# Optimization experiments

Hardware: AMD Instinct MI355X
Metric: run time of the kernel (lower is better)

## Reference

```python
import jax, jax.numpy as jnp
import numpy as np

# Graph geometry: G complete graphs (molecules) of n nodes each.
N_PER_G, G, DEG = 64, 256, 16
H, D = 8, 8
IN_DIM = H * D      # 64
EDGE_DIM = 64
N = N_PER_G * G                      # 16384 nodes
EF = G * N_PER_G * N_PER_G           # 1,048,576 full edges
ES = G * N_PER_G * DEG               # 262,144 sparse edges
SCALE = float(np.sqrt(D))


def _edges():
    n = N_PER_G
    # full graph: all (i -> j) pairs per block, edge id = b*n*n + i*n + j
    ij = np.arange(n * n)
    i, j = ij // n, ij % n
    b = np.arange(G)[:, None]
    src_full = (b * n + i[None, :]).reshape(-1).astype(np.int32)
    dst_full = (b * n + j[None, :]).reshape(-1).astype(np.int32)
    # sparse graph: each dst j receives from DEG distinct sources (j+1..j+DEG mod n)
    jj = np.arange(n)[:, None]
    kk = np.arange(DEG)[None, :]
    ii = (jj + 1 + kk) % n
    eid_block = (ii * n + jj).reshape(-1)                 # [n*DEG]
    sparse_eid = (np.arange(G)[:, None] * n * n + eid_block[None, :]).reshape(-1).astype(np.int32)
    return jnp.asarray(src_full), jnp.asarray(dst_full), jnp.asarray(sparse_eid)


def setup_inputs() -> dict:
    key = jax.random.key(0)
    ks = jax.random.split(key, 16)
    w = lambda k, shape, s=0.05: s * jax.random.normal(k, shape, jnp.float32)
    src_full, dst_full, sparse_eid = _edges()
    return dict(
        h=jax.random.normal(ks[0], (N, IN_DIM), jnp.float32),
        e=jax.random.normal(ks[1], (ES, EDGE_DIM), jnp.float32),
        adj2=jax.random.uniform(ks[2], (EF,), jnp.float32),
        rel_pos_3d=jax.random.normal(ks[3], (EF, H), jnp.float32),
        Wq=w(ks[4], (H * D, IN_DIM)), bq=jnp.zeros((H * D,), jnp.float32),
        Wk=w(ks[5], (H * D, IN_DIM)), bk=jnp.zeros((H * D,), jnp.float32),
        Wv=w(ks[6], (H * D, IN_DIM)), bv=jnp.zeros((H * D,), jnp.float32),
        Wpe=w(ks[7], (H, EDGE_DIM)), bpe=jnp.zeros((H,), jnp.float32),
        Wap=w(ks[8], (EDGE_DIM, H)), bap=jnp.zeros((EDGE_DIM,), jnp.float32),
        Wo=w(ks[9], (H * D, H * D)), bo=jnp.zeros((H * D,), jnp.float32),
        Woe=w(ks[10], (EDGE_DIM, EDGE_DIM)), boe=jnp.zeros((EDGE_DIM,), jnp.float32),
        src_full=src_full, dst_full=dst_full, sparse_eid=sparse_eid,
    )


def reference(h, e, adj2, rel_pos_3d, Wq, bq, Wk, bk, Wv, bv, Wpe, bpe,
              Wap, bap, Wo, bo, Woe, boe, src_full, dst_full, sparse_eid):
    Qh = (h @ Wq.T + bq).reshape(N, H, D)
    Kh = (h @ Wk.T + bk).reshape(N, H, D)
    Vh = (h @ Wv.T + bv).reshape(N, H, D)
    proj_e = e @ Wpe.T + bpe                                   # [ES, H]
    # edge-wise QK dot (src=K, dst=Q), scaled, then gaussian-decay + rel-pos bias
    score = jnp.sum(Kh[src_full] * Qh[dst_full], axis=-1) / SCALE   # [EF, H]
    score = score * adj2[:, None] + rel_pos_3d                      # [EF, H]
    # gather sparse-subgraph scores, project for edge output, add proj_e bias
    sc_sp = score[sparse_eid]                                        # [ES, H]
    e_out_raw = sc_sp @ Wap.T + bap                                  # [ES, EDGE_DIM]
    score = score.at[sparse_eid].set(sc_sp + proj_e)
    # edge softmax over incoming edges of each destination node
    logits = jnp.clip(score, -5.0, 5.0)
    m = jax.ops.segment_max(logits, dst_full, num_segments=N)
    ex = jnp.exp(logits - m[dst_full])
    den = jax.ops.segment_sum(ex, dst_full, num_segments=N)
    attn = ex / den[dst_full]                                        # [EF, H]
    # weighted scatter-sum of source values
    wV = jax.ops.segment_sum(Vh[src_full] * attn[..., None], dst_full, num_segments=N)
    h_out = wV.reshape(N, H * D) @ Wo.T + bo
    e_out = (e_out_raw + e) @ Woe.T + boe
    return h_out, e_out
```

## Files before the change

### kernel.cpp

```cpp
#include <hip/hip_runtime.h>


__global__ __launch_bounds__(512, 2) void qkvpe_kernel(
    const float* __restrict__ h,
    const float* __restrict__ e,
    const float* __restrict__ adj2,
    const float* __restrict__ rel,
    const float* __restrict__ Wq, const float* __restrict__ bq,
    const float* __restrict__ Wk, const float* __restrict__ bk,
    const float* __restrict__ Wv, const float* __restrict__ bv,
    const float* __restrict__ Wpe, const float* __restrict__ bpe,
    float* __restrict__ Qs, float* __restrict__ Ks, float* __restrict__ Vs,
    float* __restrict__ PEs, float* __restrict__ relT, float* __restrict__ adjT)
{
    __shared__ float shA[64 * 65];
    __shared__ float shR[8 * 576];
    const int t = threadIdx.x;
    if (blockIdx.x < 256) {
        const int b    = blockIdx.x;
        const int lane = t & 63;
        const int wu   = __builtin_amdgcn_readfirstlane(t >> 6);
        const float* hrow = h + (size_t)(b * 64 + lane) * 64;
        float accQ[8], accK[8], accV[8];
        #pragma unroll
        for (int cc = 0; cc < 8; ++cc) {
            const int c = wu * 8 + cc;
            accQ[cc] = bq[c]; accK[cc] = bk[c]; accV[cc] = bv[c];
        }
        #pragma unroll 1
        for (int k0 = 0; k0 < 4; ++k0) {
            float hv[16];
            #pragma unroll
            for (int u = 0; u < 4; ++u) {
                const float4 x = ((const float4*)hrow)[k0 * 4 + u];
                hv[u*4+0] = x.x; hv[u*4+1] = x.y; hv[u*4+2] = x.z; hv[u*4+3] = x.w;
            }
            #pragma unroll
            for (int cc = 0; cc < 8; ++cc) {
                const int c = wu * 8 + cc;
                const float* wq  = Wq + c * 64 + k0 * 16;
                const float* wk  = Wk + c * 64 + k0 * 16;
                const float* wvp = Wv + c * 64 + k0 * 16;
                #pragma unroll
                for (int k = 0; k < 16; ++k) {
                    accQ[cc] = fmaf(hv[k], wq[k],  accQ[cc]);
                    accK[cc] = fmaf(hv[k], wk[k],  accK[cc]);
                    accV[cc] = fmaf(hv[k], wvp[k], accV[cc]);
                }
            }
        }
        const size_t o = (size_t)(b * 64 + lane) * 64 + wu * 8;
        *(float4*)(Qs + o)     = make_float4(accQ[0], accQ[1], accQ[2], accQ[3]);
        *(float4*)(Qs + o + 4) = make_float4(accQ[4], accQ[5], accQ[6], accQ[7]);
        *(float4*)(Ks + o)     = make_float4(accK[0], accK[1], accK[2], accK[3]);
        *(float4*)(Ks + o + 4) = make_float4(accK[4], accK[5], accK[6], accK[7]);
        *(float4*)(Vs + o)     = make_float4(accV[0], accV[1], accV[2], accV[3]);
        *(float4*)(Vs + o + 4) = make_float4(accV[4], accV[5], accV[6], accV[7]);
    } else if (blockIdx.x < 768) {
        const int row = (blockIdx.x - 256) * 512 + t;
        const float* erow = e + (size_t)row * 64;
        float acc[8];
        #pragma unroll
        for (int h2 = 0; h2 < 8; ++h2) acc[h2] = bpe[h2];
        #pragma unroll 1
        for (int k0 = 0; k0 < 4; ++k0) {
            float ev[16];
            #pragma unroll
            for (int u = 0; u < 4; ++u) {
                const float4 x = ((const float4*)erow)[k0 * 4 + u];
                ev[u*4+0] = x.x; ev[u*4+1] = x.y; ev[u*4+2] = x.z; ev[u*4+3] = x.w;
            }
            #pragma unroll
            for (int h2 = 0; h2 < 8; ++h2) {
                const float* wp = Wpe + h2 * 64 + k0 * 16;
                #pragma unroll
                for (int k = 0; k < 16; ++k)
                    acc[h2] = fmaf(ev[k], wp[k], acc[h2]);
            }
        }
        float* p0 = PEs + (size_t)row * 8;
        *(float4*)(p0)     = make_float4(acc[0], acc[1], acc[2], acc[3]);
        *(float4*)(p0 + 4) = make_float4(acc[4], acc[5], acc[6], acc[7]);
    } else {
        const int b = blockIdx.x - 768;
        {
            const float* ap = adj2 + (size_t)b * 4096 + t * 8;
            #pragma unroll
            for (int d = 0; d < 8; ++d)
                shA[((t & 7) * 8 + d) * 65 + (t >> 3)] = ap[d];
        }
        __syncthreads();
        {
            const int j = t & 63, c = t >> 6;
            float* op = adjT + (size_t)b * 4096 + c * 512 + j * 8;
            #pragma unroll
            for (int d = 0; d < 8; ++d)
                op[d] = shA[j * 65 + c * 8 + d];
        }
        #pragma unroll 1
        for (int c = 0; c < 8; ++c) {
            __syncthreads();
            {
                const float* rp = rel + (size_t)b * 32768 + c * 4096 + t * 8;
                const int i8 = t >> 6;
                const int g  = t & 63;
                #pragma unroll
                for (int d = 0; d < 8; ++d)
                    shR[i8 * 576 + g * 9 + d] = rp[d];
            }
            __syncthreads();
            {
                float* op = relT + (size_t)b * 32768 + c * 4096 + t * 8;
                #pragma unroll
                for (int i8 = 0; i8 < 8; ++i8)
                    op[i8] = shR[i8 * 576 + (t >> 3) * 9 + (t & 7)];
            }
        }
    }
}

__global__ __launch_bounds__(256, 1) void attn_kernel(
    const float* __restrict__ Qs, const float* __restrict__ Ks,
    const float* __restrict__ Vs, const float* __restrict__ PEs,
    const float* __restrict__ adjT,
    const float* __restrict__ relT,
    float* __restrict__ wVg,
    float* __restrict__ scsp)
{
    __shared__ float shK[64 * 64];
    __shared__ float shV[64 * 64];
    __shared__ float shPE[512 * 8];
    __shared__ float shAdj[64 * 33];

    const int b2 = blockIdx.x;
    const int b  = b2 >> 1;
    const int j0 = (b2 & 1) << 5;
    const int t  = threadIdx.x;
    const int jl = t >> 3;
    const int hh = t & 7;
    const int j  = j0 + jl;

    const float* rT = relT + (size_t)b * 32768 + (size_t)j0 * 64 + t * 8;
    float R[64];
    #pragma unroll
    for (int c = 0; c < 8; ++c) {
        const float4 x = *(const float4*)(rT + c * 4096);
        const float4 y = *(const float4*)(rT + c * 4096 + 4);
        R[c*8+0] = x.x; R[c*8+1] = x.y; R[c*8+2] = x.z; R[c*8+3] = x.w;
        R[c*8+4] = y.x; R[c*8+5] = y.y; R[c*8+6] = y.z; R[c*8+7] = y.w;
    }
    {
        const float4* srcK = (const float4*)(Ks + (size_t)b * 4096);
        const float4* srcV = (const float4*)(Vs + (size_t)b * 4096);
        float4* dK = (float4*)shK; float4* dV = (float4*)shV;
        #pragma unroll
        for (int u = 0; u < 4; ++u) {
            dK[u * 256 + t] = srcK[u * 256 + t];
            dV[u * 256 + t] = srcV[u * 256 + t];
        }
        const float4* srcP = (const float4*)(PEs + ((size_t)b * 1024 + j0 * 16) * 8);
        float4* dP = (float4*)shPE;
        #pragma unroll
        for (int u = 0; u < 4; ++u)
            dP[u * 256 + t] = srcP[u * 256 + t];
    }
    {
        const int c = t >> 5, o = t & 31;
        const float4 a0 = *(const float4*)(adjT + (size_t)b * 4096 + c * 512 + (j0 + o) * 8);
        const float4 a1 = *(const float4*)(adjT + (size_t)b * 4096 + c * 512 + (j0 + o) * 8 + 4);
        shAdj[(c*8+0) * 33 + o] = a0.x; shAdj[(c*8+1) * 33 + o] = a0.y;
        shAdj[(c*8+2) * 33 + o] = a0.z; shAdj[(c*8+3) * 33 + o] = a0.w;
        shAdj[(c*8+4) * 33 + o] = a1.x; shAdj[(c*8+5) * 33 + o] = a1.y;
        shAdj[(c*8+6) * 33 + o] = a1.z; shAdj[(c*8+7) * 33 + o] = a1.w;
    }
    float q[8];
    {
        const float* qp = Qs + (size_t)(b * 64 + j) * 64 + hh * 8;
        const float4 a = *(const float4*)qp;
        const float4 c4 = *(const float4*)(qp + 4);
        q[0]=a.x; q[1]=a.y; q[2]=a.z; q[3]=a.w;
        q[4]=c4.x; q[5]=c4.y; q[6]=c4.z; q[7]=c4.w;
    }
    __syncthreads();

    float den = 0.f;
    float wv[8] = {0.f,0.f,0.f,0.f,0.f,0.f,0.f,0.f};
    const float inv_scale = 0.35355339059327379f;
    #pragma unroll
    for (int i = 0; i < 64; ++i) {
        const float4 kA = *(const float4*)&shK[i * 64 + hh * 8];
        const float4 kC = *(const float4*)&shK[i * 64 + hh * 8 + 4];
        float s = kA.x * q[0];
        s = fmaf(kA.y, q[1], s); s = fmaf(kA.z, q[2], s); s = fmaf(kA.w, q[3], s);
        s = fmaf(kC.x, q[4], s); s = fmaf(kC.y, q[5], s); s = fmaf(kC.z, q[6], s);
        s = fmaf(kC.w, q[7], s);
        s = fmaf(s * inv_scale, shAdj[i * 33 + jl], R[i]);
        const int kidx = (i - j - 1) & 63;
        if (kidx < 16) {
            const int x = (jl * 16 + kidx) * 8 + hh;
            const float pe = shPE[x];
            shPE[x] = s;
            s += pe;
        }
        s = fminf(fmaxf(s, -5.f), 5.f);
        const float ex = __expf(s);
        den += ex;
        const float4 vA = *(const float4*)&shV[i * 64 + hh * 8];
        const float4 vC = *(const float4*)&shV[i * 64 + hh * 8 + 4];
        wv[0] = fmaf(ex, vA.x, wv[0]); wv[1] = fmaf(ex, vA.y, wv[1]);
        wv[2] = fmaf(ex, vA.z, wv[2]); wv[3] = fmaf(ex, vA.w, wv[3]);
        wv[4] = fmaf(ex, vC.x, wv[4]); wv[5] = fmaf(ex, vC.y, wv[5]);
        wv[6] = fmaf(ex, vC.z, wv[6]); wv[7] = fmaf(ex, vC.w, wv[7]);
    }
    __syncthreads();

    {
        const float4* src = (const float4*)shPE;
        float4* dst = (float4*)(scsp + ((size_t)b * 1024 + j0 * 16) * 8);
        #pragma unroll
        for (int u = 0; u < 4; ++u)
            dst[u * 256 + t] = src[u * 256 + t];
    }
    const float id = 1.f / den;
    float* wp = wVg + (size_t)(b * 64 + j) * 64 + hh * 8;
    *(float4*)(wp)     = make_float4(wv[0]*id, wv[1]*id, wv[2]*id, wv[3]*id);
    *(float4*)(wp + 4) = make_float4(wv[4]*id, wv[5]*id, wv[6]*id, wv[7]*id);
}

__global__ __launch_bounds__(256, 2) void hout_kernel(
    const float* __restrict__ wVg,
    const float* __restrict__ Wo, const float* __restrict__ bo,
    float* __restrict__ h_out)
{
    __shared__ float shWT[64 * 69];
    __shared__ float shWoT[64 * 65];

    const int t    = threadIdx.x;
    const int base = blockIdx.x * 64;
    {
        const int r0 = t >> 2, qq = t & 3;
        const float* ep = wVg + (size_t)(base + r0) * 64 + qq * 16;
        #pragma unroll
        for (int v = 0; v < 4; ++v) {
            const float4 x = ((const float4*)ep)[v];
            const int c = qq * 16 + v * 4;
            shWT[(c + 0) * 69 + r0] = x.x;
            shWT[(c + 1) * 69 + r0] = x.y;
            shWT[(c + 2) * 69 + r0] = x.z;
            shWT[(c + 3) * 69 + r0] = x.w;
        }
    }
    {
        const int c0 = t >> 2, qq = t & 3;
        const float* wp = Wo + c0 * 64 + qq * 16;
        #pragma unroll
        for (int v = 0; v < 4; ++v) {
            const float4 x = ((const float4*)wp)[v];
            const int k = qq * 16 + v * 4;
            shWoT[(k + 0) * 65 + c0] = x.x;
            shWoT[(k + 1) * 65 + c0] = x.y;
            shWoT[(k + 2) * 65 + c0] = x.z;
            shWoT[(k + 3) * 65 + c0] = x.w;
        }
    }
    __syncthreads();

    const int rq = t >> 4, cq = t & 15;
    float acc[16];
    {
        const float4 bv = *(const float4*)(bo + cq * 4);
        #pragma unroll
        for (int ri = 0; ri < 4; ++ri) {
            acc[ri*4+0] = bv.x; acc[ri*4+1] = bv.y;
            acc[ri*4+2] = bv.z; acc[ri*4+3] = bv.w;
        }
    }
    #pragma unroll
    for (int k = 0; k < 64; ++k) {
        const float4 ev = *(const float4*)&shWT[k * 69 + rq * 4];
        const float4 wk = *(const float4*)&shWoT[k * 65 + cq * 4];
        acc[0]  = fmaf(ev.x, wk.x, acc[0]);  acc[1]  = fmaf(ev.x, wk.y, acc[1]);
        acc[2]  = fmaf(ev.x, wk.z, acc[2]);  acc[3]  = fmaf(ev.x, wk.w, acc[3]);
        acc[4]  = fmaf(ev.y, wk.x, acc[4]);  acc[5]  = fmaf(ev.y, wk.y, acc[5]);
        acc[6]  = fmaf(ev.y, wk.z, acc[6]);  acc[7]  = fmaf(ev.y, wk.w, acc[7]);
        acc[8]  = fmaf(ev.z, wk.x, acc[8]);  acc[9]  = fmaf(ev.z, wk.y, acc[9]);
        acc[10] = fmaf(ev.z, wk.z, acc[10]); acc[11] = fmaf(ev.z, wk.w, acc[11]);
        acc[12] = fmaf(ev.w, wk.x, acc[12]); acc[13] = fmaf(ev.w, wk.y, acc[13]);
        acc[14] = fmaf(ev.w, wk.z, acc[14]); acc[15] = fmaf(ev.w, wk.w, acc[15]);
    }
    #pragma unroll
    for (int ri = 0; ri < 4; ++ri) {
        float* orow = h_out + (size_t)(base + rq * 4 + ri) * 64 + cq * 4;
        *(float4*)orow = make_float4(acc[ri*4+0], acc[ri*4+1], acc[ri*4+2], acc[ri*4+3]);
    }
}

__global__ void prep_kernel(const float* __restrict__ Wap, const float* __restrict__ bap,
                            const float* __restrict__ Woe, const float* __restrict__ boe,
                            float* __restrict__ M2, float* __restrict__ Tm, int hasT)
{
    const int tg = blockIdx.x * 64 + threadIdx.x;
    if (tg < 512) {
        const int c = tg >> 3, hq = tg & 7;
        float s = 0.f;
        #pragma unroll 8
        for (int k = 0; k < 64; ++k) s = fmaf(Woe[c * 64 + k], Wap[k * 8 + hq], s);
        M2[tg] = s;
    } else if (tg < 576) {
        const int c = tg - 512;
        float s = boe[c];
        #pragma unroll 8
        for (int k = 0; k < 64; ++k) s = fmaf(bap[k], Woe[c * 64 + k], s);
        M2[512 + c] = s;
    } else if (hasT && tg < 576 + 73 * 64) {
        const int idx = tg - 576;
        const int k = idx >> 6, c = idx & 63;
        float v;
        if (k < 64) {
            v = Woe[c * 64 + k];
        } else if (k < 72) {
            const int hq = k - 64;
            v = 0.f;
            #pragma unroll 8
            for (int kk = 0; kk < 64; ++kk)
                v = fmaf(Woe[c * 64 + kk], Wap[kk * 8 + hq], v);
        } else {
            v = boe[c];
            #pragma unroll 8
            for (int kk = 0; kk < 64; ++kk)
                v = fmaf(bap[kk], Woe[c * 64 + kk], v);
        }
        Tm[k * 64 + c] = v;
    }
}

__global__ __launch_bounds__(256, 2) void eoutT_kernel(
    const float* __restrict__ e,
    const float* __restrict__ scsp,
    const float* __restrict__ Tm,
    float* __restrict__ e_out)
{
    const int t   = threadIdx.x;
    const int r   = t & 63;
    const int w   = __builtin_amdgcn_readfirstlane(t >> 6);
    const int row = blockIdx.x * 64 + r;

    float ev[72];
    {
        const float* ep = e + (size_t)row * 64;
        #pragma unroll
        for (int v = 0; v < 16; ++v) {
            const float4 x = ((const float4*)ep)[v];
            ev[v*4+0] = x.x; ev[v*4+1] = x.y; ev[v*4+2] = x.z; ev[v*4+3] = x.w;
        }
        const float4 s0 = *(const float4*)(scsp + (size_t)row * 8);
        const float4 s1 = *(const float4*)(scsp + (size_t)row * 8 + 4);
        ev[64]=s0.x; ev[65]=s0.y; ev[66]=s0.z; ev[67]=s0.w;
        ev[68]=s1.x; ev[69]=s1.y; ev[70]=s1.z; ev[71]=s1.w;
    }
    const float* wbase = Tm + w * 16;
    float acc[16];
    #pragma unroll
    for (int u = 0; u < 16; ++u) acc[u] = wbase[72 * 64 + u];
    #pragma unroll
    for (int k = 0; k < 72; ++k) {
        const float* wk = wbase + k * 64;
        #pragma unroll
        for (int u = 0; u < 16; ++u)
            acc[u] = fmaf(ev[k], wk[u], acc[u]);
    }
    float* orow = e_out + (size_t)row * 64 + w * 16;
    #pragma unroll
    for (int u = 0; u < 4; ++u)
        *(float4*)&orow[u * 4] =
            make_float4(acc[u*4+0], acc[u*4+1], acc[u*4+2], acc[u*4+3]);
}

__global__ __launch_bounds__(256, 2) void eout_kernel(
    const float* __restrict__ e,
    const float* __restrict__ scsp,
    const float* __restrict__ Woe,
    const float* __restrict__ M2g,
    float* __restrict__ e_out)
{
    __shared__ float shE[64 * 64];
    __shared__ float shS[64 * 8];
    const int t    = threadIdx.x;
    const int base = blockIdx.x * 64;
    {
        const int r = t >> 2, qq = t & 3;
        const float* ep = e + (size_t)(base + r) * 64 + qq * 16;
        #pragma unroll
        for (int u = 0; u < 4; ++u) {
            const float4 x = ((const float4*)ep)[u];
            const int cc = qq * 4 + u;
            *(float4*)&shE[r * 64 + ((cc ^ (r & 15)) << 2)] = x;
        }
    }
    if (t < 128) {
        const int r = t >> 1, pp = t & 1;
        *(float4*)&shS[r * 8 + pp * 4] =
            *(const float4*)(scsp + (size_t)(base + r) * 8 + pp * 4);
    }
    __syncthreads();
    const int w = __builtin_amdgcn_readfirstlane(t >> 6);
    const int r = t & 63;
    float sc[8];
    {
        const float4 a  = *(const float4*)&shS[r * 8];
        const float4 c4 = *(const float4*)&shS[r * 8 + 4];
        sc[0]=a.x; sc[1]=a.y; sc[2]=a.z; sc[3]=a.w;
        sc[4]=c4.x; sc[5]=c4.y; sc[6]=c4.z; sc[7]=c4.w;
    }
    float acc[16];
    #pragma unroll
    for (int u = 0; u < 16; ++u) {
        const int c = w * 16 + u;
        float s = M2g[512 + c];
        #pragma unroll
        for (int hq = 0; hq < 8; ++hq)
            s = fmaf(sc[hq], M2g[c * 8 + hq], s);
        acc[u] = s;
    }
    #pragma unroll
    for (int k0 = 0; k0 < 4; ++k0) {
        float ev[16];
        #pragma unroll
        for (int v = 0; v < 4; ++v) {
            const int cc = k0 * 4 + v;
            const float4 x = *(const float4*)&shE[r * 64 + ((cc ^ (r & 15)) << 2)];
            ev[v*4+0] = x.x; ev[v*4+1] = x.y; ev[v*4+2] = x.z; ev[v*4+3] = x.w;
        }
        #pragma unroll
        for (int u = 0; u < 16; ++u) {
            const float* wr = Woe + (w * 16 + u) * 64 + k0 * 16;
            #pragma unroll
            for (int k = 0; k < 16; ++k)
                acc[u] = fmaf(ev[k], wr[k], acc[u]);
        }
    }
    float* orow = e_out + (size_t)(base + r) * 64 + w * 16;
    #pragma unroll
    for (int u = 0; u < 4; ++u)
        *(float4*)&orow[u * 4] =
            make_float4(acc[u*4+0], acc[u*4+1], acc[u*4+2], acc[u*4+3]);
}

extern "C" void kernel_launch(void* const* d_in, const int* in_sizes, int n_in,
                              void* d_out, int out_size, void* d_ws, size_t ws_size,
                              hipStream_t stream) {
    const float* h    = (const float*)d_in[0];
    const float* e    = (const float*)d_in[1];
    const float* adj2 = (const float*)d_in[2];
    const float* rel  = (const float*)d_in[3];
    const float* Wq   = (const float*)d_in[4];  const float* bq  = (const float*)d_in[5];
    const float* Wk   = (const float*)d_in[6];  const float* bk  = (const float*)d_in[7];
    const float* Wv   = (const float*)d_in[8];  const float* bv  = (const float*)d_in[9];
    const float* Wpe  = (const float*)d_in[10]; const float* bpe = (const float*)d_in[11];
    const float* Wap  = (const float*)d_in[12]; const float* bap = (const float*)d_in[13];
    const float* Wo   = (const float*)d_in[14]; const float* bo  = (const float*)d_in[15];
    const float* Woe  = (const float*)d_in[16]; const float* boe = (const float*)d_in[17];

    float* out  = (float*)d_out;
    float* hout = out;
    float* eout = out + 16384 * 64;
    float* Qs   = eout;
    float* Ks   = eout + 1048576;
    float* Vs   = eout + 2097152;
    float* PEs  = eout + 3145728;
    float* relT = eout + 5242880;
    float* adjT = eout + 13631488;
    float* ws   = (float*)d_ws;
    float* scsp = ws;
    float* M2g  = ws + 2097152;
    float* Tm   = ws + 2098176;
    const int hasT = (ws_size >= (size_t)(2098176 + 73 * 64) * sizeof(float)) ? 1 : 0;

    prep_kernel<<<dim3(82), dim3(64), 0, stream>>>(Wap, bap, Woe, boe, M2g, Tm, hasT);
    qkvpe_kernel<<<dim3(1024), dim3(512), 0, stream>>>(
        h, e, adj2, rel, Wq, bq, Wk, bk, Wv, bv, Wpe, bpe,
        Qs, Ks, Vs, PEs, relT, adjT);
    attn_kernel<<<dim3(512), dim3(256), 0, stream>>>(
        Qs, Ks, Vs, PEs, adjT, relT, hout , scsp);
    hout_kernel<<<dim3(256), dim3(256), 0, stream>>>(hout, Wo, bo, hout);
    if (hasT)
        eoutT_kernel<<<dim3(4096), dim3(256), 0, stream>>>(e, scsp, Tm, eout);
    else
        eout_kernel<<<dim3(4096), dim3(256), 0, stream>>>(e, scsp, Woe, M2g, eout);
}
```

Before: 145.7 us.

## Read adj2 and rel_pos directly in attention kernel, drop transpose pass

```diff
diff --git a/kernel.cpp b/kernel.cpp
--- a/kernel.cpp
+++ b/kernel.cpp
@@ -4,17 +4,13 @@
 __global__ __launch_bounds__(512, 2) void qkvpe_kernel(
     const float* __restrict__ h,
     const float* __restrict__ e,
-    const float* __restrict__ adj2,
-    const float* __restrict__ rel,
     const float* __restrict__ Wq, const float* __restrict__ bq,
     const float* __restrict__ Wk, const float* __restrict__ bk,
     const float* __restrict__ Wv, const float* __restrict__ bv,
     const float* __restrict__ Wpe, const float* __restrict__ bpe,
     float* __restrict__ Qs, float* __restrict__ Ks, float* __restrict__ Vs,
-    float* __restrict__ PEs, float* __restrict__ relT, float* __restrict__ adjT)
-{
-    __shared__ float shA[64 * 65];
-    __shared__ float shR[8 * 576];
+    float* __restrict__ PEs)
+{
     const int t = threadIdx.x;
     if (blockIdx.x < 256) {
         const int b    = blockIdx.x;
@@ -56,7 +52,7 @@
         *(float4*)(Ks + o + 4) = make_float4(accK[4], accK[5], accK[6], accK[7]);
         *(float4*)(Vs + o)     = make_float4(accV[0], accV[1], accV[2], accV[3]);
         *(float4*)(Vs + o + 4) = make_float4(accV[4], accV[5], accV[6], accV[7]);
-    } else if (blockIdx.x < 768) {
+    } else {
         const int row = (blockIdx.x - 256) * 512 + t;
         const float* erow = e + (size_t)row * 64;
         float acc[8];
@@ -81,49 +77,14 @@
         float* p0 = PEs + (size_t)row * 8;
         *(float4*)(p0)     = make_float4(acc[0], acc[1], acc[2], acc[3]);
         *(float4*)(p0 + 4) = make_float4(acc[4], acc[5], acc[6], acc[7]);
-    } else {
-        const int b = blockIdx.x - 768;
-        {
-            const float* ap = adj2 + (size_t)b * 4096 + t * 8;
-            #pragma unroll
-            for (int d = 0; d < 8; ++d)
-                shA[((t & 7) * 8 + d) * 65 + (t >> 3)] = ap[d];
-        }
-        __syncthreads();
-        {
-            const int j = t & 63, c = t >> 6;
-            float* op = adjT + (size_t)b * 4096 + c * 512 + j * 8;
-            #pragma unroll
-            for (int d = 0; d < 8; ++d)
-                op[d] = shA[j * 65 + c * 8 + d];
-        }
-        #pragma unroll 1
-        for (int c = 0; c < 8; ++c) {
-            __syncthreads();
-            {
-                const float* rp = rel + (size_t)b * 32768 + c * 4096 + t * 8;
-                const int i8 = t >> 6;
-                const int g  = t & 63;
-                #pragma unroll
-                for (int d = 0; d < 8; ++d)
-                    shR[i8 * 576 + g * 9 + d] = rp[d];
-            }
-            __syncthreads();
-            {
-                float* op = relT + (size_t)b * 32768 + c * 4096 + t * 8;
-                #pragma unroll
-                for (int i8 = 0; i8 < 8; ++i8)
-                    op[i8] = shR[i8 * 576 + (t >> 3) * 9 + (t & 7)];
-            }
-        }
     }
 }
 
 __global__ __launch_bounds__(256, 1) void attn_kernel(
     const float* __restrict__ Qs, const float* __restrict__ Ks,
     const float* __restrict__ Vs, const float* __restrict__ PEs,
-    const float* __restrict__ adjT,
-    const float* __restrict__ relT,
+    const float* __restrict__ adj2,
+    const float* __restrict__ rel,
     float* __restrict__ wVg,
     float* __restrict__ scsp)
 {
@@ -140,15 +101,12 @@
     const int hh = t & 7;
     const int j  = j0 + jl;
 
-    const float* rT = relT + (size_t)b * 32768 + (size_t)j0 * 64 + t * 8;
+    const float* relBase = rel + (size_t)b * 32768 + j0 * 8 + t;
     float R[64];
     #pragma unroll
-    for (int c = 0; c < 8; ++c) {
-        const float4 x = *(const float4*)(rT + c * 4096);
-        const float4 y = *(const float4*)(rT + c * 4096 + 4);
-        R[c*8+0] = x.x; R[c*8+1] = x.y; R[c*8+2] = x.z; R[c*8+3] = x.w;
-        R[c*8+4] = y.x; R[c*8+5] = y.y; R[c*8+6] = y.z; R[c*8+7] = y.w;
-    }
+    for (int i = 0; i < 64; ++i)
+        R[i] = relBase[(size_t)i * 512];
+
     {
         const float4* srcK = (const float4*)(Ks + (size_t)b * 4096);
         const float4* srcV = (const float4*)(Vs + (size_t)b * 4096);
@@ -165,13 +123,13 @@
             dP[u * 256 + t] = srcP[u * 256 + t];
     }
     {
-        const int c = t >> 5, o = t & 31;
-        const float4 a0 = *(const float4*)(adjT + (size_t)b * 4096 + c * 512 + (j0 + o) * 8);
-        const float4 a1 = *(const float4*)(adjT + (size_t)b * 4096 + c * 512 + (j0 + o) * 8 + 4);
-        shAdj[(c*8+0) * 33 + o] = a0.x; shAdj[(c*8+1) * 33 + o] = a0.y;
-        shAdj[(c*8+2) * 33 + o] = a0.z; shAdj[(c*8+3) * 33 + o] = a0.w;
-        shAdj[(c*8+4) * 33 + o] = a1.x; shAdj[(c*8+5) * 33 + o] = a1.y;
-        shAdj[(c*8+6) * 33 + o] = a1.z; shAdj[(c*8+7) * 33 + o] = a1.w;
+        const int i2 = t >> 2, grp = t & 3;
+        const float* ap = adj2 + (size_t)b * 4096 + i2 * 64 + j0 + grp * 8;
+        const float4 a0 = *(const float4*)(ap);
+        const float4 a1 = *(const float4*)(ap + 4);
+        float* dp = &shAdj[i2 * 33 + grp * 8];
+        dp[0] = a0.x; dp[1] = a0.y; dp[2] = a0.z; dp[3] = a0.w;
+        dp[4] = a1.x; dp[5] = a1.y; dp[6] = a1.z; dp[7] = a1.w;
     }
     float q[8];
     {
@@ -468,8 +426,6 @@
     float* Ks   = eout + 1048576;
     float* Vs   = eout + 2097152;
     float* PEs  = eout + 3145728;
-    float* relT = eout + 5242880;
-    float* adjT = eout + 13631488;
     float* ws   = (float*)d_ws;
     float* scsp = ws;
     float* M2g  = ws + 2097152;
@@ -477,11 +433,10 @@
     const int hasT = (ws_size >= (size_t)(2098176 + 73 * 64) * sizeof(float)) ? 1 : 0;
 
     prep_kernel<<<dim3(82), dim3(64), 0, stream>>>(Wap, bap, Woe, boe, M2g, Tm, hasT);
-    qkvpe_kernel<<<dim3(1024), dim3(512), 0, stream>>>(
-        h, e, adj2, rel, Wq, bq, Wk, bk, Wv, bv, Wpe, bpe,
-        Qs, Ks, Vs, PEs, relT, adjT);
+    qkvpe_kernel<<<dim3(768), dim3(512), 0, stream>>>(
+        h, e, Wq, bq, Wk, bk, Wv, bv, Wpe, bpe, Qs, Ks, Vs, PEs);
     attn_kernel<<<dim3(512), dim3(256), 0, stream>>>(
-        Qs, Ks, Vs, PEs, adjT, relT, hout , scsp);
+        Qs, Ks, Vs, PEs, adj2, rel, hout , scsp);
     hout_kernel<<<dim3(256), dim3(256), 0, stream>>>(hout, Wo, bo, hout);
     if (hasT)
         eoutT_kernel<<<dim3(4096), dim3(256), 0, stream>>>(e, scsp, Tm, eout);
```

After: 142.9 us. No clear change (-1.9%).
